# Kernel optimization log

Hardware: AMD Instinct MI355X
Metric: run time of the kernel (lower is better)

The kernel has to match this reference:

```python
import jax, jax.numpy as jnp
import numpy as np

B, L, DM, H, PD = 2, 1024, 512, 8, 64
D = DM // H  # head_dim = 64
NEG = -10000.0


def setup_inputs() -> dict:
    key = jax.random.key(0)
    ks = jax.random.split(key, 12)
    s = 1.0 / np.sqrt(DM)
    sp = 1.0 / np.sqrt(PD)
    return {
        "x": jax.random.normal(ks[0], (B, L, DM), dtype=jnp.float32),
        "z": jax.random.normal(ks[1], (B, L, L, PD), dtype=jnp.float32),
        "residue_mask": jnp.ones((B, L), dtype=bool),
        "Wq": jax.random.normal(ks[2], (DM, DM), dtype=jnp.float32) * s,
        "bq": jnp.zeros((DM,), dtype=jnp.float32),
        "Wk": jax.random.normal(ks[3], (DM, DM), dtype=jnp.float32) * s,
        "bk": jnp.zeros((DM,), dtype=jnp.float32),
        "Wv": jax.random.normal(ks[4], (DM, DM), dtype=jnp.float32) * s,
        "bv": jnp.zeros((DM,), dtype=jnp.float32),
        "Wo": jax.random.normal(ks[5], (DM, DM), dtype=jnp.float32) * s,
        "bo": jnp.zeros((DM,), dtype=jnp.float32),
        "Wpb": jax.random.normal(ks[6], (PD, H), dtype=jnp.float32) * sp,
    }


def reference(x, z, residue_mask, Wq, bq, Wk, bk, Wv, bv, Wo, bo, Wpb):
    b, l, c = x.shape
    scale = 1.0 / np.sqrt(D)
    # projections -> (B, H, L, D)
    q = (x @ Wq + bq).reshape(b, l, H, D).transpose(0, 2, 1, 3)
    k = (x @ Wk + bk).reshape(b, l, H, D).transpose(0, 2, 1, 3)
    v = (x @ Wv + bv).reshape(b, l, H, D).transpose(0, 2, 1, 3)
    # pair bias: (B, L, L, PD) @ (PD, H) -> (B, H, L, L)
    bias = jnp.einsum('bijp,ph->bhij', z, Wpb)
    logits = jnp.einsum('bhid,bhjd->bhij', q, k) * scale + bias
    key_ok = residue_mask[:, None, None, :]
    query_ok = residue_mask[:, None, :, None]
    logits = jnp.where(key_ok, logits, NEG)
    logits = jnp.where(query_ok, logits, NEG)
    attn = jax.nn.softmax(logits, axis=-1)
    out = jnp.einsum('bhij,bhjd->bhid', attn, v)
    out = out.transpose(0, 2, 1, 3).reshape(b, l, c)
    return out @ Wo + bo
```

## Files before the change

### kernel.cpp

```cpp
#include <hip/hip_runtime.h>

typedef __bf16 bf16;
typedef __attribute__((ext_vector_type(4))) __bf16 bf16x4;
typedef __attribute__((ext_vector_type(8))) __bf16 bf16x8;
typedef __attribute__((ext_vector_type(4))) float f32x4;
typedef __attribute__((ext_vector_type(4))) _Float16 f16x4;

#define B_   2
#define L_   1024
#define DM_  512
#define H_   8
#define D_   64
#define PD_  64
#define NEG_VAL -10000.0f

#define XB_N   (2048*512)
#define WT_N   (1536*512)
#define WTO_N  (512*512)
#define WTPB_N (16*64)

static __device__ __forceinline__ f32x4 mfma_bf16(bf16x8 a, bf16x8 b, f32x4 c) {
  return __builtin_amdgcn_mfma_f32_16x16x32_bf16(a, b, c, 0, 0, 0);
}

__global__ __launch_bounds__(256) void prep_kernel(
    const float* __restrict__ x, const float* __restrict__ Wq, const float* __restrict__ Wk,
    const float* __restrict__ Wv, const float* __restrict__ Wo, const float* __restrict__ Wpb,
    bf16* __restrict__ xb, bf16* __restrict__ Wt, bf16* __restrict__ Wto, bf16* __restrict__ Wtpb) {
  const int total = XB_N + WT_N + WTO_N + WTPB_N;
  for (int idx = blockIdx.x * 256 + threadIdx.x; idx < total; idx += gridDim.x * 256) {
    if (idx < XB_N) {
      xb[idx] = (bf16)x[idx];
    } else if (idx < XB_N + WT_N) {
      int t = idx - XB_N;
      int n = t >> 9, kk = t & 511;
      int sel = n >> 9, nn = n & 511;
      const float* W = sel == 0 ? Wq : (sel == 1 ? Wk : Wv);
      Wt[t] = (bf16)W[kk * 512 + nn];
    } else if (idx < XB_N + WT_N + WTO_N) {
      int t = idx - XB_N - WT_N;
      int n = t >> 9, kk = t & 511;
      Wto[t] = (bf16)Wo[kk * 512 + n];
    } else {
      int t = idx - XB_N - WT_N - WTO_N;
      int n = t >> 6, kk = t & 63;
      Wtpb[t] = (n < 8) ? (bf16)Wpb[kk * 8 + n] : (bf16)0.0f;
    }
  }
}

__global__ __launch_bounds__(256) void qkv_gemm(
    const bf16* __restrict__ xb, const bf16* __restrict__ Wt,
    const float* __restrict__ bq, const float* __restrict__ bk, const float* __restrict__ bv,
    bf16* __restrict__ qb, bf16* __restrict__ kb, bf16* __restrict__ vT) {
  int wid = blockIdx.x * 4 + (threadIdx.x >> 6);
  int lane = threadIdx.x & 63;
  int mt = wid / 48, nt = wid - mt * 48;
  int row0 = mt * 32, col0 = nt * 32;
  int lr = lane & 15, lg = lane >> 4;
  const bf16* a0p = xb + (row0 + lr) * 512 + lg * 8;
  const bf16* a1p = a0p + 16 * 512;
  const bf16* b0p = Wt + (col0 + lr) * 512 + lg * 8;
  const bf16* b1p = b0p + 16 * 512;
  f32x4 acc00 = {0.f,0.f,0.f,0.f}, acc01 = acc00, acc10 = acc00, acc11 = acc00;
#pragma unroll
  for (int kk = 0; kk < 512; kk += 32) {
    bf16x8 a0 = *reinterpret_cast<const bf16x8*>(a0p + kk);
    bf16x8 a1 = *reinterpret_cast<const bf16x8*>(a1p + kk);
    bf16x8 b0 = *reinterpret_cast<const bf16x8*>(b0p + kk);
    bf16x8 b1 = *reinterpret_cast<const bf16x8*>(b1p + kk);
    acc00 = mfma_bf16(a0, b0, acc00);
    acc01 = mfma_bf16(a0, b1, acc01);
    acc10 = mfma_bf16(a1, b0, acc10);
    acc11 = mfma_bf16(a1, b1, acc11);
  }
#pragma unroll
  for (int ni = 0; ni < 2; ++ni) {
    int col = col0 + ni * 16 + lr;
    int wsel = col >> 9;
    int ncol = col & 511;
    int h = ncol >> 6, d = ncol & 63;
    const float* bias = wsel == 0 ? bq : (wsel == 1 ? bk : bv);
    float bval = bias[ncol];
#pragma unroll
    for (int mi = 0; mi < 2; ++mi) {
      f32x4 acc = (mi == 0) ? (ni == 0 ? acc00 : acc01) : (ni == 0 ? acc10 : acc11);
      int m0 = row0 + mi * 16 + lg * 4;
      int bidx = m0 >> 10, l0 = m0 & 1023;
      if (wsel == 2) {
        bf16x4 pv;
#pragma unroll
        for (int r = 0; r < 4; ++r) pv[r] = (bf16)(acc[r] + bval);
        *reinterpret_cast<bf16x4*>(vT + ((long)(bidx * H_ + h) * D_ + d) * L_ + l0) = pv;
      } else if (wsel == 0) {
#pragma unroll
        for (int r = 0; r < 4; ++r)
          qb[((long)(bidx * H_ + h) * L_ + l0 + r) * D_ + d] = (bf16)((acc[r] + bval) * 0.125f);
      } else {
#pragma unroll
        for (int r = 0; r < 4; ++r)
          kb[((long)(bidx * H_ + h) * L_ + l0 + r) * D_ + d] = (bf16)(acc[r] + bval);
      }
    }
  }
}

__global__ __launch_bounds__(256) void bias_gemm(
    const float* __restrict__ z, const bf16* __restrict__ Wtpb, _Float16* __restrict__ biasbuf) {
  int wid = blockIdx.x * 4 + (threadIdx.x >> 6);
  int lane = threadIdx.x & 63;
  int lr = lane & 15, lg = lane >> 4;
  long p0 = (long)wid * 16;
  const float* zr = z + (p0 + lr) * 64;
  f32x4 z0 = *reinterpret_cast<const f32x4*>(zr + lg * 8);
  f32x4 z1 = *reinterpret_cast<const f32x4*>(zr + lg * 8 + 4);
  f32x4 z2 = *reinterpret_cast<const f32x4*>(zr + 32 + lg * 8);
  f32x4 z3 = *reinterpret_cast<const f32x4*>(zr + 32 + lg * 8 + 4);
  bf16x8 a0, a1;
#pragma unroll
  for (int e = 0; e < 4; ++e) { a0[e] = (bf16)z0[e]; a0[e + 4] = (bf16)z1[e]; }
#pragma unroll
  for (int e = 0; e < 4; ++e) { a1[e] = (bf16)z2[e]; a1[e + 4] = (bf16)z3[e]; }
  bf16x8 b0 = *reinterpret_cast<const bf16x8*>(Wtpb + lr * 64 + lg * 8);
  bf16x8 b1 = *reinterpret_cast<const bf16x8*>(Wtpb + lr * 64 + 32 + lg * 8);
  f32x4 acc = {0.f, 0.f, 0.f, 0.f};
  acc = mfma_bf16(a0, b0, acc);
  acc = mfma_bf16(a1, b1, acc);
  if (lr < 8) {
    int h = lr;
    int bidx = (int)(p0 >> 20);
    int i = ((int)(p0 >> 10)) & 1023;
    int j = ((int)p0 & 1023) + lg * 4;
    _Float16* dst = biasbuf + ((((long)bidx * H_ + h) * L_ + i) << 10) + j;
    f16x4 hv;
#pragma unroll
    for (int r = 0; r < 4; ++r) hv[r] = (_Float16)acc[r];
    *reinterpret_cast<f16x4*>(dst) = hv;
  }
}

__global__ __launch_bounds__(256) void attn_kernel(
    const bf16* __restrict__ qb, const bf16* __restrict__ kb, const bf16* __restrict__ vT,
    const _Float16* __restrict__ biasbuf, const int* __restrict__ mask, bf16* __restrict__ attn_out) {
  __shared__ bf16  p_lds[4][16][64];
  __shared__ float o_lds[4][16][64];
  __shared__ float m_lds[4][16];
  __shared__ float l_lds[4][16];
  int bid = blockIdx.x;
  int b = bid >> 9, h = (bid >> 6) & 7, it = bid & 63;
  int i0 = it * 16;
  int tid = threadIdx.x, w = tid >> 6, lane = tid & 63, lr = lane & 15, lg = lane >> 4;

  const bf16* qrow = qb + ((long)(b * H_ + h) * L_ + i0 + lr) * D_ + lg * 8;
  bf16x8 qa0 = *reinterpret_cast<const bf16x8*>(qrow);
  bf16x8 qa1 = *reinterpret_cast<const bf16x8*>(qrow + 32);
  const bf16* kbase = kb + (long)(b * H_ + h) * L_ * D_;
  const bf16* vbase = vT + (long)(b * H_ + h) * D_ * L_;
  const _Float16* bias_base = biasbuf + ((long)(b * H_ + h) * L_ + i0) * L_;
  const int* mrow_mask = mask + b * L_;

  bool qok[4];
#pragma unroll
  for (int r = 0; r < 4; ++r) qok[r] = mrow_mask[i0 + lg * 4 + r] != 0;

  float mr[4] = {-3.0e38f, -3.0e38f, -3.0e38f, -3.0e38f};
  float lsum[4] = {0.f, 0.f, 0.f, 0.f};
  f32x4 o0 = {0.f,0.f,0.f,0.f}, o1 = o0, o2 = o0, o3 = o0;

  char* p_base = (char*)&p_lds[w][0][0];

  for (int jt = 0; jt < 4; ++jt) {
    int j0 = w * 256 + jt * 64;
    f32x4 s0, s1, s2, s3;
#pragma unroll
    for (int jsub = 0; jsub < 4; ++jsub) {
      int j = j0 + jsub * 16 + lr;
      f32x4 acc;
#pragma unroll
      for (int r = 0; r < 4; ++r) acc[r] = (float)bias_base[(long)(lg * 4 + r) * L_ + j];
      const bf16* kr = kbase + (long)j * D_ + lg * 8;
      acc = mfma_bf16(qa0, *reinterpret_cast<const bf16x8*>(kr), acc);
      acc = mfma_bf16(qa1, *reinterpret_cast<const bf16x8*>(kr + 32), acc);
      bool kok = mrow_mask[j] != 0;
      if (!kok) {
#pragma unroll
        for (int r = 0; r < 4; ++r) acc[r] = NEG_VAL;
      }
      if (jsub == 0) s0 = acc; else if (jsub == 1) s1 = acc; else if (jsub == 2) s2 = acc; else s3 = acc;
    }
#pragma unroll
    for (int r = 0; r < 4; ++r) {
      if (!qok[r]) { s0[r] = NEG_VAL; s1[r] = NEG_VAL; s2[r] = NEG_VAL; s3[r] = NEG_VAL; }
    }
#pragma unroll
    for (int r = 0; r < 4; ++r) {
      float mt_ = fmaxf(fmaxf(s0[r], s1[r]), fmaxf(s2[r], s3[r]));
#pragma unroll
      for (int off = 1; off <= 8; off <<= 1) mt_ = fmaxf(mt_, __shfl_xor(mt_, off));
      float mnew = fmaxf(mr[r], mt_);
      float alpha = __expf(mr[r] - mnew);
      mr[r] = mnew;
      float p0 = __expf(s0[r] - mnew);
      float p1 = __expf(s1[r] - mnew);
      float p2 = __expf(s2[r] - mnew);
      float p3 = __expf(s3[r] - mnew);
      float ps = p0 + p1 + p2 + p3;
#pragma unroll
      for (int off = 1; off <= 8; off <<= 1) ps += __shfl_xor(ps, off);
      lsum[r] = lsum[r] * alpha + ps;
      o0[r] *= alpha; o1[r] *= alpha; o2[r] *= alpha; o3[r] *= alpha;
      int row = lg * 4 + r;
      int sw = (row & 7) << 4;
      *(bf16*)(p_base + row * 128 + ((lr * 2) ^ sw)) = (bf16)p0;
      *(bf16*)(p_base + row * 128 + ((32 + lr * 2) ^ sw)) = (bf16)p1;
      *(bf16*)(p_base + row * 128 + ((64 + lr * 2) ^ sw)) = (bf16)p2;
      *(bf16*)(p_base + row * 128 + ((96 + lr * 2) ^ sw)) = (bf16)p3;
    }
    int swr = (lr & 7) << 4;
    bf16x8 pa0 = *(const bf16x8*)(p_base + lr * 128 + ((lg * 16) ^ swr));
    bf16x8 pa1 = *(const bf16x8*)(p_base + lr * 128 + ((64 + lg * 16) ^ swr));
#pragma unroll
    for (int dsub = 0; dsub < 4; ++dsub) {
      const bf16* vr = vbase + (long)(dsub * 16 + lr) * L_ + j0 + lg * 8;
      bf16x8 vb0 = *reinterpret_cast<const bf16x8*>(vr);
      bf16x8 vb1 = *reinterpret_cast<const bf16x8*>(vr + 32);
      f32x4 acc = (dsub == 0) ? o0 : (dsub == 1) ? o1 : (dsub == 2) ? o2 : o3;
      acc = mfma_bf16(pa0, vb0, acc);
      acc = mfma_bf16(pa1, vb1, acc);
      if (dsub == 0) o0 = acc; else if (dsub == 1) o1 = acc; else if (dsub == 2) o2 = acc; else o3 = acc;
    }
  }
#pragma unroll
  for (int r = 0; r < 4; ++r) {
    int row = lg * 4 + r;
    o_lds[w][row][0 * 16 + lr] = o0[r];
    o_lds[w][row][1 * 16 + lr] = o1[r];
    o_lds[w][row][2 * 16 + lr] = o2[r];
    o_lds[w][row][3 * 16 + lr] = o3[r];
    if (lr == 0) { m_lds[w][row] = mr[r]; l_lds[w][row] = lsum[r]; }
  }
  __syncthreads();
  {
    int row = tid >> 4, d0 = (tid & 15) * 4;
    float M = fmaxf(fmaxf(m_lds[0][row], m_lds[1][row]), fmaxf(m_lds[2][row], m_lds[3][row]));
    float lt = 0.f;
    float oacc[4] = {0.f, 0.f, 0.f, 0.f};
#pragma unroll
    for (int ww = 0; ww < 4; ++ww) {
      float c = __expf(m_lds[ww][row] - M);
      lt += c * l_lds[ww][row];
#pragma unroll
      for (int e = 0; e < 4; ++e) oacc[e] += c * o_lds[ww][row][d0 + e];
    }
    float inv = 1.0f / lt;
    bf16x4 ov;
#pragma unroll
    for (int e = 0; e < 4; ++e) ov[e] = (bf16)(oacc[e] * inv);
    *reinterpret_cast<bf16x4*>(attn_out + ((long)(b * L_ + i0 + row)) * DM_ + h * D_ + d0) = ov;
  }
}

__global__ __launch_bounds__(256) void out_gemm(
    const bf16* __restrict__ ab, const bf16* __restrict__ Wto,
    const float* __restrict__ bo, float* __restrict__ out) {
  int wid = blockIdx.x * 4 + (threadIdx.x >> 6);
  int lane = threadIdx.x & 63;
  int mt = wid >> 4, nt = wid & 15;
  int row0 = mt * 32, col0 = nt * 32;
  int lr = lane & 15, lg = lane >> 4;
  const bf16* a0p = ab + (row0 + lr) * 512 + lg * 8;
  const bf16* a1p = a0p + 16 * 512;
  const bf16* b0p = Wto + (col0 + lr) * 512 + lg * 8;
  const bf16* b1p = b0p + 16 * 512;
  f32x4 acc00 = {0.f,0.f,0.f,0.f}, acc01 = acc00, acc10 = acc00, acc11 = acc00;
#pragma unroll
  for (int kk = 0; kk < 512; kk += 32) {
    bf16x8 a0 = *reinterpret_cast<const bf16x8*>(a0p + kk);
    bf16x8 a1 = *reinterpret_cast<const bf16x8*>(a1p + kk);
    bf16x8 b0 = *reinterpret_cast<const bf16x8*>(b0p + kk);
    bf16x8 b1 = *reinterpret_cast<const bf16x8*>(b1p + kk);
    acc00 = mfma_bf16(a0, b0, acc00);
    acc01 = mfma_bf16(a0, b1, acc01);
    acc10 = mfma_bf16(a1, b0, acc10);
    acc11 = mfma_bf16(a1, b1, acc11);
  }
#pragma unroll
  for (int ni = 0; ni < 2; ++ni) {
    int col = col0 + ni * 16 + lr;
    float bval = bo[col];
#pragma unroll
    for (int mi = 0; mi < 2; ++mi) {
      f32x4 acc = (mi == 0) ? (ni == 0 ? acc00 : acc01) : (ni == 0 ? acc10 : acc11);
      int m0 = row0 + mi * 16 + lg * 4;
#pragma unroll
      for (int r = 0; r < 4; ++r) out[(long)(m0 + r) * 512 + col] = acc[r] + bval;
    }
  }
}

extern "C" void kernel_launch(void* const* d_in, const int* in_sizes, int n_in,
                              void* d_out, int out_size, void* d_ws, size_t ws_size,
                              hipStream_t stream) {
  const float* x    = (const float*)d_in[0];
  const float* z    = (const float*)d_in[1];
  const int*   mask = (const int*)d_in[2];
  const float* Wq   = (const float*)d_in[3];
  const float* bq   = (const float*)d_in[4];
  const float* Wk   = (const float*)d_in[5];
  const float* bk   = (const float*)d_in[6];
  const float* Wv   = (const float*)d_in[7];
  const float* bv   = (const float*)d_in[8];
  const float* Wo   = (const float*)d_in[9];
  const float* bo   = (const float*)d_in[10];
  const float* Wpb  = (const float*)d_in[11];

  char* ws = (char*)d_ws;
  bf16* xb        = (bf16*)(ws + 0);
  bf16* Wt        = (bf16*)(ws + 2097152);
  bf16* Wto       = (bf16*)(ws + 3670016);
  bf16* Wtpb      = (bf16*)(ws + 4194304);
  bf16* qbuf      = (bf16*)(ws + 4196352);
  bf16* kbuf      = (bf16*)(ws + 6293504);
  bf16* vTbuf     = (bf16*)(ws + 8390656);
  bf16* attn_out  = (bf16*)(ws + 10487808);
  _Float16* biasb = (_Float16*)(ws + 12584960);

  prep_kernel<<<2048, 256, 0, stream>>>(x, Wq, Wk, Wv, Wo, Wpb, xb, Wt, Wto, Wtpb);
  qkv_gemm<<<768, 256, 0, stream>>>(xb, Wt, bq, bk, bv, qbuf, kbuf, vTbuf);
  bias_gemm<<<32768, 256, 0, stream>>>(z, Wtpb, biasb);
  attn_kernel<<<1024, 256, 0, stream>>>(qbuf, kbuf, vTbuf, biasb, mask, attn_out);
  out_gemm<<<256, 256, 0, stream>>>(attn_out, Wto, bo, (float*)d_out);
}
```

Baseline: 212.7 us.

## Fuse pair-bias projection into attention with split-K partials and merge kernel

Removes the separate bias_gemm and its fp16 bias buffer. The attention kernel now projects z through Wpb on the fly into LDS for a 16-row by 64-column tile covering all 8 heads. Each block handles one query tile and one quarter of the keys, with each wave covering two heads. Partial O, m and l values go to global memory, and a new merge kernel combines them. This avoids writing and re-reading the 32 MB bias tensor, at the cost of extra partial-output traffic, two block-wide barriers per tile, and only 512 blocks streaming the 512 MB of z.

```diff
diff --git a/kernel.cpp b/kernel.cpp
--- a/kernel.cpp
+++ b/kernel.cpp
@@ -4,7 +4,6 @@
 typedef __attribute__((ext_vector_type(4))) __bf16 bf16x4;
 typedef __attribute__((ext_vector_type(8))) __bf16 bf16x8;
 typedef __attribute__((ext_vector_type(4))) float f32x4;
-typedef __attribute__((ext_vector_type(4))) _Float16 f16x4;
 
 #define B_   2
 #define L_   1024
@@ -105,159 +104,200 @@
   }
 }
 
-__global__ __launch_bounds__(256) void bias_gemm(
-    const float* __restrict__ z, const bf16* __restrict__ Wtpb, _Float16* __restrict__ biasbuf) {
-  int wid = blockIdx.x * 4 + (threadIdx.x >> 6);
-  int lane = threadIdx.x & 63;
-  int lr = lane & 15, lg = lane >> 4;
-  long p0 = (long)wid * 16;
-  const float* zr = z + (p0 + lr) * 64;
-  f32x4 z0 = *reinterpret_cast<const f32x4*>(zr + lg * 8);
-  f32x4 z1 = *reinterpret_cast<const f32x4*>(zr + lg * 8 + 4);
-  f32x4 z2 = *reinterpret_cast<const f32x4*>(zr + 32 + lg * 8);
-  f32x4 z3 = *reinterpret_cast<const f32x4*>(zr + 32 + lg * 8 + 4);
-  bf16x8 a0, a1;
-#pragma unroll
-  for (int e = 0; e < 4; ++e) { a0[e] = (bf16)z0[e]; a0[e + 4] = (bf16)z1[e]; }
-#pragma unroll
-  for (int e = 0; e < 4; ++e) { a1[e] = (bf16)z2[e]; a1[e + 4] = (bf16)z3[e]; }
-  bf16x8 b0 = *reinterpret_cast<const bf16x8*>(Wtpb + lr * 64 + lg * 8);
-  bf16x8 b1 = *reinterpret_cast<const bf16x8*>(Wtpb + lr * 64 + 32 + lg * 8);
-  f32x4 acc = {0.f, 0.f, 0.f, 0.f};
-  acc = mfma_bf16(a0, b0, acc);
-  acc = mfma_bf16(a1, b1, acc);
-  if (lr < 8) {
-    int h = lr;
-    int bidx = (int)(p0 >> 20);
-    int i = ((int)(p0 >> 10)) & 1023;
-    int j = ((int)p0 & 1023) + lg * 4;
-    _Float16* dst = biasbuf + ((((long)bidx * H_ + h) * L_ + i) << 10) + j;
-    f16x4 hv;
-#pragma unroll
-    for (int r = 0; r < 4; ++r) hv[r] = (_Float16)acc[r];
-    *reinterpret_cast<f16x4*>(dst) = hv;
-  }
-}
-
-__global__ __launch_bounds__(256) void attn_kernel(
-    const bf16* __restrict__ qb, const bf16* __restrict__ kb, const bf16* __restrict__ vT,
-    const _Float16* __restrict__ biasbuf, const int* __restrict__ mask, bf16* __restrict__ attn_out) {
-  __shared__ bf16  p_lds[4][16][64];
-  __shared__ float o_lds[4][16][64];
-  __shared__ float m_lds[4][16];
-  __shared__ float l_lds[4][16];
+__global__ __launch_bounds__(256) void fused_attn(
+    const float* __restrict__ z, const bf16* __restrict__ qb, const bf16* __restrict__ kb,
+    const bf16* __restrict__ vT, const bf16* __restrict__ Wtpb, const int* __restrict__ mask,
+    float* __restrict__ part_o, float* __restrict__ part_m, float* __restrict__ part_l) {
+  __shared__ _Float16 bias_lds[8 * 16 * 64];
+  __shared__ bf16 p_lds_raw[8][16 * 64];
   int bid = blockIdx.x;
-  int b = bid >> 9, h = (bid >> 6) & 7, it = bid & 63;
-  int i0 = it * 16;
+  int jc = bid & 3, it = (bid >> 2) & 63, b = bid >> 8;
+  int i0 = it * 16, jb = jc * 256;
   int tid = threadIdx.x, w = tid >> 6, lane = tid & 63, lr = lane & 15, lg = lane >> 4;
 
-  const bf16* qrow = qb + ((long)(b * H_ + h) * L_ + i0 + lr) * D_ + lg * 8;
-  bf16x8 qa0 = *reinterpret_cast<const bf16x8*>(qrow);
-  bf16x8 qa1 = *reinterpret_cast<const bf16x8*>(qrow + 32);
-  const bf16* kbase = kb + (long)(b * H_ + h) * L_ * D_;
-  const bf16* vbase = vT + (long)(b * H_ + h) * D_ * L_;
-  const _Float16* bias_base = biasbuf + ((long)(b * H_ + h) * L_ + i0) * L_;
-  const int* mrow_mask = mask + b * L_;
-
+  bf16x8 wpb0 = *reinterpret_cast<const bf16x8*>(Wtpb + lr * 64 + lg * 8);
+  bf16x8 wpb1 = *reinterpret_cast<const bf16x8*>(Wtpb + lr * 64 + 32 + lg * 8);
+
+  const bf16* q0p = qb + ((long)(b * H_ + w * 2 + 0) * L_ + i0 + lr) * D_ + lg * 8;
+  const bf16* q1p = qb + ((long)(b * H_ + w * 2 + 1) * L_ + i0 + lr) * D_ + lg * 8;
+  bf16x8 qa00 = *reinterpret_cast<const bf16x8*>(q0p);
+  bf16x8 qa01 = *reinterpret_cast<const bf16x8*>(q0p + 32);
+  bf16x8 qa10 = *reinterpret_cast<const bf16x8*>(q1p);
+  bf16x8 qa11 = *reinterpret_cast<const bf16x8*>(q1p + 32);
+
+  const int* mrow = mask + b * L_;
   bool qok[4];
 #pragma unroll
-  for (int r = 0; r < 4; ++r) qok[r] = mrow_mask[i0 + lg * 4 + r] != 0;
-
-  float mr[4] = {-3.0e38f, -3.0e38f, -3.0e38f, -3.0e38f};
-  float lsum[4] = {0.f, 0.f, 0.f, 0.f};
-  f32x4 o0 = {0.f,0.f,0.f,0.f}, o1 = o0, o2 = o0, o3 = o0;
-
-  char* p_base = (char*)&p_lds[w][0][0];
-
-  for (int jt = 0; jt < 4; ++jt) {
-    int j0 = w * 256 + jt * 64;
-    f32x4 s0, s1, s2, s3;
-#pragma unroll
-    for (int jsub = 0; jsub < 4; ++jsub) {
-      int j = j0 + jsub * 16 + lr;
-      f32x4 acc;
-#pragma unroll
-      for (int r = 0; r < 4; ++r) acc[r] = (float)bias_base[(long)(lg * 4 + r) * L_ + j];
-      const bf16* kr = kbase + (long)j * D_ + lg * 8;
-      acc = mfma_bf16(qa0, *reinterpret_cast<const bf16x8*>(kr), acc);
-      acc = mfma_bf16(qa1, *reinterpret_cast<const bf16x8*>(kr + 32), acc);
-      bool kok = mrow_mask[j] != 0;
-      if (!kok) {
-#pragma unroll
-        for (int r = 0; r < 4; ++r) acc[r] = NEG_VAL;
-      }
-      if (jsub == 0) s0 = acc; else if (jsub == 1) s1 = acc; else if (jsub == 2) s2 = acc; else s3 = acc;
-    }
+  for (int r = 0; r < 4; ++r) qok[r] = mrow[i0 + lg * 4 + r] != 0;
+
+  float mr[2][4], ls[2][4];
+  f32x4 o[2][4];
+#pragma unroll
+  for (int hh = 0; hh < 2; ++hh)
 #pragma unroll
     for (int r = 0; r < 4; ++r) {
-      if (!qok[r]) { s0[r] = NEG_VAL; s1[r] = NEG_VAL; s2[r] = NEG_VAL; s3[r] = NEG_VAL; }
-    }
-#pragma unroll
-    for (int r = 0; r < 4; ++r) {
-      float mt_ = fmaxf(fmaxf(s0[r], s1[r]), fmaxf(s2[r], s3[r]));
-#pragma unroll
-      for (int off = 1; off <= 8; off <<= 1) mt_ = fmaxf(mt_, __shfl_xor(mt_, off));
-      float mnew = fmaxf(mr[r], mt_);
-      float alpha = __expf(mr[r] - mnew);
-      mr[r] = mnew;
-      float p0 = __expf(s0[r] - mnew);
-      float p1 = __expf(s1[r] - mnew);
-      float p2 = __expf(s2[r] - mnew);
-      float p3 = __expf(s3[r] - mnew);
-      float ps = p0 + p1 + p2 + p3;
-#pragma unroll
-      for (int off = 1; off <= 8; off <<= 1) ps += __shfl_xor(ps, off);
-      lsum[r] = lsum[r] * alpha + ps;
-      o0[r] *= alpha; o1[r] *= alpha; o2[r] *= alpha; o3[r] *= alpha;
-      int row = lg * 4 + r;
-      int sw = (row & 7) << 4;
-      *(bf16*)(p_base + row * 128 + ((lr * 2) ^ sw)) = (bf16)p0;
-      *(bf16*)(p_base + row * 128 + ((32 + lr * 2) ^ sw)) = (bf16)p1;
-      *(bf16*)(p_base + row * 128 + ((64 + lr * 2) ^ sw)) = (bf16)p2;
-      *(bf16*)(p_base + row * 128 + ((96 + lr * 2) ^ sw)) = (bf16)p3;
-    }
-    int swr = (lr & 7) << 4;
-    bf16x8 pa0 = *(const bf16x8*)(p_base + lr * 128 + ((lg * 16) ^ swr));
-    bf16x8 pa1 = *(const bf16x8*)(p_base + lr * 128 + ((64 + lg * 16) ^ swr));
-#pragma unroll
-    for (int dsub = 0; dsub < 4; ++dsub) {
-      const bf16* vr = vbase + (long)(dsub * 16 + lr) * L_ + j0 + lg * 8;
-      bf16x8 vb0 = *reinterpret_cast<const bf16x8*>(vr);
-      bf16x8 vb1 = *reinterpret_cast<const bf16x8*>(vr + 32);
-      f32x4 acc = (dsub == 0) ? o0 : (dsub == 1) ? o1 : (dsub == 2) ? o2 : o3;
-      acc = mfma_bf16(pa0, vb0, acc);
-      acc = mfma_bf16(pa1, vb1, acc);
-      if (dsub == 0) o0 = acc; else if (dsub == 1) o1 = acc; else if (dsub == 2) o2 = acc; else o3 = acc;
-    }
-  }
-#pragma unroll
-  for (int r = 0; r < 4; ++r) {
-    int row = lg * 4 + r;
-    o_lds[w][row][0 * 16 + lr] = o0[r];
-    o_lds[w][row][1 * 16 + lr] = o1[r];
-    o_lds[w][row][2 * 16 + lr] = o2[r];
-    o_lds[w][row][3 * 16 + lr] = o3[r];
-    if (lr == 0) { m_lds[w][row] = mr[r]; l_lds[w][row] = lsum[r]; }
-  }
-  __syncthreads();
-  {
-    int row = tid >> 4, d0 = (tid & 15) * 4;
-    float M = fmaxf(fmaxf(m_lds[0][row], m_lds[1][row]), fmaxf(m_lds[2][row], m_lds[3][row]));
-    float lt = 0.f;
-    float oacc[4] = {0.f, 0.f, 0.f, 0.f};
-#pragma unroll
-    for (int ww = 0; ww < 4; ++ww) {
-      float c = __expf(m_lds[ww][row] - M);
-      lt += c * l_lds[ww][row];
-#pragma unroll
-      for (int e = 0; e < 4; ++e) oacc[e] += c * o_lds[ww][row][d0 + e];
-    }
-    float inv = 1.0f / lt;
-    bf16x4 ov;
-#pragma unroll
-    for (int e = 0; e < 4; ++e) ov[e] = (bf16)(oacc[e] * inv);
-    *reinterpret_cast<bf16x4*>(attn_out + ((long)(b * L_ + i0 + row)) * DM_ + h * D_ + d0) = ov;
-  }
+      mr[hh][r] = -3.0e38f; ls[hh][r] = 0.f;
+      o[hh][r] = f32x4{0.f, 0.f, 0.f, 0.f};
+    }
+
+  for (int t = 0; t < 4; ++t) {
+    int j64 = jb + t * 64;
+    {
+      char* bl = (char*)bias_lds;
+      int xo = (lr << 4) ^ (w << 5);
+#pragma unroll
+      for (int ii = 0; ii < 4; ++ii) {
+        int i = w * 4 + ii;
+        const float* zb_ = z + ((long)(b * L_ + i0 + i) * L_ + j64) * 64;
+#pragma unroll
+        for (int js = 0; js < 4; ++js) {
+          const float* zr = zb_ + (js * 16 + lr) * 64 + lg * 8;
+          f32x4 f0 = *reinterpret_cast<const f32x4*>(zr);
+          f32x4 f1 = *reinterpret_cast<const f32x4*>(zr + 4);
+          f32x4 f2 = *reinterpret_cast<const f32x4*>(zr + 32);
+          f32x4 f3 = *reinterpret_cast<const f32x4*>(zr + 36);
+          bf16x8 a0, a1;
+#pragma unroll
+          for (int e = 0; e < 4; ++e) {
+            a0[e] = (bf16)f0[e]; a0[e + 4] = (bf16)f1[e];
+            a1[e] = (bf16)f2[e]; a1[e + 4] = (bf16)f3[e];
+          }
+          f32x4 c = {0.f, 0.f, 0.f, 0.f};
+          c = mfma_bf16(a0, wpb0, c);
+          c = mfma_bf16(a1, wpb1, c);
+          if (lr < 8) {
+            int base = lr * 2048 + i * 128;
+#pragma unroll
+            for (int r = 0; r < 4; ++r) {
+              int jl2 = (js * 16 + lg * 4 + r) * 2;
+              *(_Float16*)(bl + base + (jl2 ^ xo)) = (_Float16)c[r];
+            }
+          }
+        }
+      }
+    }
+    __syncthreads();
+#pragma unroll
+    for (int hh = 0; hh < 2; ++hh) {
+      int h = w * 2 + hh;
+      const char* bl = (const char*)bias_lds;
+      f32x4 s0, s1, s2, s3;
+#pragma unroll
+      for (int js = 0; js < 4; ++js) {
+        int j = j64 + js * 16 + lr;
+        f32x4 acc;
+#pragma unroll
+        for (int r = 0; r < 4; ++r) {
+          int i = lg * 4 + r;
+          int byte = h * 2048 + i * 128 + ((((js * 16 + lr) * 2)) ^ (h << 4) ^ (lg << 5));
+          acc[r] = (float)*(const _Float16*)(bl + byte);
+        }
+        const bf16* kr = kb + ((long)(b * H_ + h) * L_ + j) * D_ + lg * 8;
+        bf16x8 qf0 = hh == 0 ? qa00 : qa10;
+        bf16x8 qf1 = hh == 0 ? qa01 : qa11;
+        acc = mfma_bf16(qf0, *reinterpret_cast<const bf16x8*>(kr), acc);
+        acc = mfma_bf16(qf1, *reinterpret_cast<const bf16x8*>(kr + 32), acc);
+        if (mrow[j] == 0) {
+#pragma unroll
+          for (int r = 0; r < 4; ++r) acc[r] = NEG_VAL;
+        }
+        if (js == 0) s0 = acc; else if (js == 1) s1 = acc; else if (js == 2) s2 = acc; else s3 = acc;
+      }
+#pragma unroll
+      for (int r = 0; r < 4; ++r)
+        if (!qok[r]) { s0[r] = NEG_VAL; s1[r] = NEG_VAL; s2[r] = NEG_VAL; s3[r] = NEG_VAL; }
+      char* pb = (char*)&p_lds_raw[w * 2 + hh][0];
+#pragma unroll
+      for (int r = 0; r < 4; ++r) {
+        float mt_ = fmaxf(fmaxf(s0[r], s1[r]), fmaxf(s2[r], s3[r]));
+#pragma unroll
+        for (int off = 1; off <= 8; off <<= 1) mt_ = fmaxf(mt_, __shfl_xor(mt_, off));
+        float mnew = fmaxf(mr[hh][r], mt_);
+        float alpha = __expf(mr[hh][r] - mnew);
+        mr[hh][r] = mnew;
+        float p0 = __expf(s0[r] - mnew);
+        float p1 = __expf(s1[r] - mnew);
+        float p2 = __expf(s2[r] - mnew);
+        float p3 = __expf(s3[r] - mnew);
+        float ps = p0 + p1 + p2 + p3;
+#pragma unroll
+        for (int off = 1; off <= 8; off <<= 1) ps += __shfl_xor(ps, off);
+        ls[hh][r] = ls[hh][r] * alpha + ps;
+        o[hh][0][r] *= alpha; o[hh][1][r] *= alpha; o[hh][2][r] *= alpha; o[hh][3][r] *= alpha;
+        int row = lg * 4 + r;
+        int sw = (row & 7) << 4;
+        *(bf16*)(pb + row * 128 + ((lr * 2) ^ sw)) = (bf16)p0;
+        *(bf16*)(pb + row * 128 + ((32 + lr * 2) ^ sw)) = (bf16)p1;
+        *(bf16*)(pb + row * 128 + ((64 + lr * 2) ^ sw)) = (bf16)p2;
+        *(bf16*)(pb + row * 128 + ((96 + lr * 2) ^ sw)) = (bf16)p3;
+      }
+      int swr = (lr & 7) << 4;
+      bf16x8 pa0 = *(const bf16x8*)(pb + lr * 128 + ((lg * 16) ^ swr));
+      bf16x8 pa1 = *(const bf16x8*)(pb + lr * 128 + ((64 + lg * 16) ^ swr));
+      const bf16* vbb = vT + (long)(b * H_ + h) * D_ * L_;
+#pragma unroll
+      for (int ds_ = 0; ds_ < 4; ++ds_) {
+        const bf16* vr = vbb + (long)(ds_ * 16 + lr) * L_ + j64 + lg * 8;
+        f32x4 acc = o[hh][ds_];
+        acc = mfma_bf16(pa0, *reinterpret_cast<const bf16x8*>(vr), acc);
+        acc = mfma_bf16(pa1, *reinterpret_cast<const bf16x8*>(vr + 32), acc);
+        o[hh][ds_] = acc;
+      }
+    }
+    __syncthreads();
+  }
+#pragma unroll
+  for (int hh = 0; hh < 2; ++hh) {
+    int h = w * 2 + hh;
+    long ob = ((long)bid * H_ + h) * 16;
+#pragma unroll
+    for (int ds_ = 0; ds_ < 4; ++ds_)
+#pragma unroll
+      for (int r = 0; r < 4; ++r)
+        part_o[(ob + lg * 4 + r) * 64 + ds_ * 16 + lr] = o[hh][ds_][r];
+    if (lr == 0) {
+#pragma unroll
+      for (int r = 0; r < 4; ++r) {
+        part_m[ob + lg * 4 + r] = mr[hh][r];
+        part_l[ob + lg * 4 + r] = ls[hh][r];
+      }
+    }
+  }
+}
+
+__global__ __launch_bounds__(256) void merge_kernel(
+    const float* __restrict__ part_o, const float* __restrict__ part_m,
+    const float* __restrict__ part_l, bf16* __restrict__ attn_out) {
+  int t = blockIdx.x * 256 + threadIdx.x;
+  int d0 = (t & 15) * 4;
+  int row = t >> 4;
+  int b = row >> 13, h = (row >> 10) & 7, i = row & 1023;
+  int it = i >> 4, il = i & 15;
+  float mv[4];
+  float M = -3.0e38f;
+#pragma unroll
+  for (int jcx = 0; jcx < 4; ++jcx) {
+    int bid = (b * 64 + it) * 4 + jcx;
+    mv[jcx] = part_m[((long)bid * H_ + h) * 16 + il];
+    M = fmaxf(M, mv[jcx]);
+  }
+  float lt = 0.f;
+  float oa[4] = {0.f, 0.f, 0.f, 0.f};
+#pragma unroll
+  for (int jcx = 0; jcx < 4; ++jcx) {
+    int bid = (b * 64 + it) * 4 + jcx;
+    long base = (long)bid * H_ * 16 + (long)h * 16 + il;
+    float c = __expf(mv[jcx] - M);
+    lt += c * part_l[base];
+    f32x4 ov = *reinterpret_cast<const f32x4*>(part_o + base * 64 + d0);
+#pragma unroll
+    for (int e = 0; e < 4; ++e) oa[e] += c * ov[e];
+  }
+  float inv = 1.0f / lt;
+  bf16x4 r_;
+#pragma unroll
+  for (int e = 0; e < 4; ++e) r_[e] = (bf16)(oa[e] * inv);
+  *reinterpret_cast<bf16x4*>(attn_out + ((long)(b * L_ + i)) * DM_ + h * D_ + d0) = r_;
 }
 
 __global__ __launch_bounds__(256) void out_gemm(
@@ -323,11 +363,13 @@
   bf16* kbuf      = (bf16*)(ws + 6293504);
   bf16* vTbuf     = (bf16*)(ws + 8390656);
   bf16* attn_out  = (bf16*)(ws + 10487808);
-  _Float16* biasb = (_Float16*)(ws + 12584960);
+  float* part_o   = (float*)(ws + 12584960);
+  float* part_m   = (float*)(ws + 29362176);
+  float* part_l   = (float*)(ws + 29624320);
 
   prep_kernel<<<2048, 256, 0, stream>>>(x, Wq, Wk, Wv, Wo, Wpb, xb, Wt, Wto, Wtpb);
   qkv_gemm<<<768, 256, 0, stream>>>(xb, Wt, bq, bk, bv, qbuf, kbuf, vTbuf);
-  bias_gemm<<<32768, 256, 0, stream>>>(z, Wtpb, biasb);
-  attn_kernel<<<1024, 256, 0, stream>>>(qbuf, kbuf, vTbuf, biasb, mask, attn_out);
+  fused_attn<<<512, 256, 0, stream>>>(z, qbuf, kbuf, vTbuf, Wtpb, mask, part_o, part_m, part_l);
+  merge_kernel<<<1024, 256, 0, stream>>>(part_o, part_m, part_l, attn_out);
   out_gemm<<<256, 256, 0, stream>>>(attn_out, Wto, bo, (float*)d_out);
 }
```

Measured after the change: 189.7 us. 10.8% less time.
